# Kernel tuning notes

Hardware: AMD Instinct MI355X
Metric: run time of the kernel (lower is better)

Reference implementation:

```python
import jax, jax.numpy as jnp
import numpy as np

B, D, H, W, C = 1, 6, 128, 128, 180
NH = 6
HD = C // NH
SCALE = HD ** -0.5
WS = (2, 8, 8)
SS = (1, 4, 4)
N = WS[0] * WS[1] * WS[2]  # 128 tokens per 3D window
HID = int(C * 2.0)  # GEGLU hidden = 360


def _rel_pos_index(ws):
    d, h, w = np.meshgrid(np.arange(ws[0]), np.arange(ws[1]), np.arange(ws[2]), indexing='ij')
    coords = np.stack([d, h, w]).reshape(3, -1)  # (3, N)
    rel = (coords[:, :, None] - coords[:, None, :]).transpose(1, 2, 0).astype(np.int64)
    rel[:, :, 0] += ws[0] - 1
    rel[:, :, 1] += ws[1] - 1
    rel[:, :, 2] += ws[2] - 1
    rel[:, :, 0] *= (2 * ws[1] - 1) * (2 * ws[2] - 1)
    rel[:, :, 1] *= (2 * ws[2] - 1)
    return rel.sum(-1).astype(np.int32)  # (N, N)


def _sine_pos(hw, nf, temperature=10000.0):
    scale = 2.0 * np.pi
    ones = np.ones((1, hw[0], hw[1]), np.float64)
    y = np.cumsum(ones, 1)
    x = np.cumsum(ones, 2)
    eps = 1e-6
    y = y / (y[:, -1:, :] + eps) * scale
    x = x / (x[:, :, -1:] + eps) * scale
    dim_t = temperature ** (2 * (np.arange(nf) // 2) / nf)
    px = x[..., None] / dim_t
    py = y[..., None] / dim_t
    px = np.stack([np.sin(px[..., 0::2]), np.cos(px[..., 1::2])], -1).reshape(1, hw[0], hw[1], -1)
    py = np.stack([np.sin(py[..., 0::2]), np.cos(py[..., 1::2])], -1).reshape(1, hw[0], hw[1], -1)
    pos = np.concatenate([py, px], -1)  # (1, H, W, 2*nf)
    return pos.reshape(1, hw[0] * hw[1], -1).astype(np.float32)


def _compute_mask():
    img = np.zeros((1, D, H, W, 1), np.float32)
    cnt = 0
    sl = lambda w, s: (slice(0, -w), slice(-w, -s), slice(-s, None))
    for ds in sl(WS[0], SS[0]):
        for hs in sl(WS[1], SS[1]):
            for ws_ in sl(WS[2], SS[2]):
                img[:, ds, hs, ws_, :] = cnt
                cnt += 1
    mw = img.reshape(1, D // WS[0], WS[0], H // WS[1], WS[1], W // WS[2], WS[2], 1)
    mw = mw.transpose(0, 1, 3, 5, 2, 4, 6, 7).reshape(-1, N)
    am = mw[:, None, :] - mw[:, :, None]
    return np.where(am != 0, -100.0, 0.0).astype(np.float32)  # (nW, N, N)


def win_part(x):
    b = x.shape[0]
    x = x.reshape(b, D // WS[0], WS[0], H // WS[1], WS[1], W // WS[2], WS[2], C)
    return x.transpose(0, 1, 3, 5, 2, 4, 6, 7).reshape(-1, N, C)


def win_rev(w, b):
    x = w.reshape(b, D // WS[0], H // WS[1], W // WS[2], WS[0], WS[1], WS[2], C)
    return x.transpose(0, 1, 4, 2, 5, 3, 6, 7).reshape(b, D, H, W, C)


def ln(x, g, b):
    m = x.mean(-1, keepdims=True)
    v = ((x - m) ** 2).mean(-1, keepdims=True)
    return (x - m) / jnp.sqrt(v + 1e-5) * g + b


def attn_fn(q, k, v, bias, mask):
    # q,k,v: (B_, NH, n, HD); bias: (NH, n, n) or None; mask: (nW, n, n) or None
    a = jnp.einsum('bhnd,bhmd->bhnm', q * SCALE, k)
    if bias is not None:
        a = a + bias[None]
    if mask is not None:
        nW = mask.shape[0]
        a = a.reshape(-1, nW, NH, a.shape[-2], a.shape[-1]) + mask[None, :, None]
        a = a.reshape(-1, NH, a.shape[-2], a.shape[-1])
    a = jax.nn.softmax(a, axis=-1)
    o = jnp.einsum('bhnm,bhmd->bhnd', a, v)
    return o.transpose(0, 2, 1, 3).reshape(o.shape[0], o.shape[2], -1)


def setup_inputs() -> dict:
    key = jax.random.key(0)
    ks = jax.random.split(key, 9)
    p = lambda k, shape: jax.random.normal(k, shape, jnp.float32) * 0.02
    return {
        'x': jax.random.normal(ks[0], (B, D, H, W, C), jnp.float32),
        'mask': jnp.asarray(_compute_mask()),
        'g1': jnp.ones((C,), jnp.float32), 'b1': jnp.zeros((C,), jnp.float32),
        'g2': jnp.ones((C,), jnp.float32), 'b2': jnp.zeros((C,), jnp.float32),
        'w_qkv_self': p(ks[1], (C, 3 * C)), 'b_qkv_self': jnp.zeros((3 * C,), jnp.float32),
        'w_qkv_mut': p(ks[2], (C, 3 * C)), 'b_qkv_mut': jnp.zeros((3 * C,), jnp.float32),
        'rpb_table': p(ks[3], ((2 * WS[0] - 1) * (2 * WS[1] - 1) * (2 * WS[2] - 1), NH)),
        'pos_bias': jnp.asarray(_sine_pos((WS[1], WS[2]), C // 2)),
        'w_proj': p(ks[4], (2 * C, C)), 'b_proj': jnp.zeros((C,), jnp.float32),
        'w_fc11': p(ks[5], (C, HID)), 'b_fc11': jnp.zeros((HID,), jnp.float32),
        'w_fc12': p(ks[6], (C, HID)), 'b_fc12': jnp.zeros((HID,), jnp.float32),
        'w_fc2': p(ks[7], (HID, C)), 'b_fc2': jnp.zeros((C,), jnp.float32),
        'rpi': jnp.asarray(_rel_pos_index(WS)),
    }


def reference(x, mask, g1, b1, g2, b2, w_qkv_self, b_qkv_self, w_qkv_mut, b_qkv_mut,
              rpb_table, pos_bias, w_proj, b_proj, w_fc11, b_fc11, w_fc12, b_fc12,
              w_fc2, b_fc2, rpi):
    # --- attention branch ---
    h = ln(x, g1, b1)
    h = jnp.roll(h, (-SS[0], -SS[1], -SS[2]), axis=(1, 2, 3))  # cyclic shift
    xw = win_part(h)  # (B*nW, N, C)
    B_ = xw.shape[0]

    def qkv(xin, wq, bq):
        t = (xin @ wq + bq).reshape(B_, -1, 3, NH, HD).transpose(2, 0, 3, 1, 4)
        return t[0], t[1], t[2]

    q, k, v = qkv(xw, w_qkv_self, b_qkv_self)
    bias = rpb_table[rpi.reshape(-1)].reshape(N, N, NH).transpose(2, 0, 1)
    x_self = attn_fn(q, k, v, bias, mask)

    # mutual attention between the two frames of each window
    pb = jnp.concatenate([pos_bias, pos_bias], axis=1)  # (1, N, C)
    qm, km, vm = qkv(xw + pb, w_qkv_mut, b_qkv_mut)
    half = N // 2
    q1, q2 = qm[:, :, :half], qm[:, :, half:]
    k1, k2 = km[:, :, :half], km[:, :, half:]
    v1, v2 = vm[:, :, :half], vm[:, :, half:]
    m2 = mask[:, :half, :half]
    x1 = attn_fn(q2, k1, v1, None, m2)
    x2 = attn_fn(q1, k2, v2, None, m2)
    xo = jnp.concatenate([jnp.concatenate([x1, x2], axis=1), x_self], axis=2)  # (B_, N, 2C)
    xo = xo @ w_proj + b_proj
    out = win_rev(xo, x.shape[0])
    out = jnp.roll(out, (SS[0], SS[1], SS[2]), axis=(1, 2, 3))
    x = x + out

    # --- GEGLU MLP branch ---
    h = ln(x, g2, b2)
    h = jax.nn.gelu(h @ w_fc11 + b_fc11, approximate=False) * (h @ w_fc12 + b_fc12)
    x = x + (h @ w_fc2 + b_fc2)
    return x
```

## Files before the change

### kernel.cpp

```cpp
#include <hip/hip_runtime.h>
#include <hip/hip_bf16.h>
#include <math.h>
#include <cstdio>


typedef __hip_bfloat16 bf16;
typedef __attribute__((ext_vector_type(8))) short short8;
typedef __attribute__((ext_vector_type(4))) unsigned short us4;
typedef __attribute__((ext_vector_type(4))) float f32x4;

#define SCALE_F 0.18257418583505536f
#define SZPE 18874368u

__device__ __forceinline__ bf16  f2b(float v){ return __float2bfloat16(v); }
__device__ __forceinline__ float bu2f(unsigned short u){
    union { unsigned int i; float f; } x; x.i = ((unsigned int)u) << 16; return x.f;
}
__device__ __forceinline__ f32x4 mfma16(short8 a, short8 b, f32x4 c){
    return __builtin_amdgcn_mfma_f32_16x16x32_bf16(a, b, c, 0, 0, 0);
}

__device__ __forceinline__ void gld16(const bf16* g, bf16* s){
    __builtin_amdgcn_global_load_lds(
        (const __attribute__((address_space(1))) unsigned int*)g,
        (__attribute__((address_space(3))) unsigned int*)s, 16, 0, 0);
}

__device__ __forceinline__ int xswz(){
    return (blockIdx.x & 7) * ((int)gridDim.x >> 3) + ((int)blockIdx.x >> 3);
}

__device__ __forceinline__ int wincnt(int win, int tok){
    int d = (win >> 8) * 2 + (tok >> 6);
    int h = ((win >> 4) & 15) * 8 + ((tok >> 3) & 7);
    int w = (win & 15) * 8 + (tok & 7);
    int rd = (d >= 4) + (d >= 5);
    int rh = (h >= 120) + (h >= 124);
    int rw = (w >= 120) + (w >= 124);
    return (rd * 3 + rh) * 3 + rw;
}

__global__ __launch_bounds__(256) void k_pack_qkv(const float* __restrict__ w,
                                                  const float* __restrict__ bias,
                                                  bf16* __restrict__ Bt,
                                                  float* __restrict__ bb)
{
    int idx = blockIdx.x * 256 + threadIdx.x;
    int n = idx / 192, k = idx - n * 192;
    int three = n / 192;
    int rem = n - three * 192, nh = rem >> 5, hdp = rem & 31;
    int srcc = three * 180 + nh * 30 + hdp;
    float v = 0.f;
    if (hdp < 30 && k < 180) v = w[(size_t)k * 540 + srcc];
    if (three == 0) v *= SCALE_F;
    Bt[(size_t)n * 192 + k] = f2b(v);
    if (k == 0) bb[n] = (hdp < 30) ? ((three == 0 ? SCALE_F : 1.f) * bias[srcc]) : 0.f;
}

__global__ __launch_bounds__(256) void k_pack(const float* __restrict__ w,
                                              int NW, int K, int KP,
                                              bf16* __restrict__ Bt)
{
    int idx = blockIdx.x * 256 + threadIdx.x;
    int n = idx / KP, k = idx - n * KP;
    float v = (n < NW && k < K) ? w[(size_t)k * NW + n] : 0.f;
    Bt[idx] = f2b(v);
}

__global__ __launch_bounds__(256) void k_rpbg(const float* __restrict__ rpb,
                                              const int* __restrict__ rpi,
                                              bf16* __restrict__ biasrT)
{
    int n = blockIdx.x * 256 + threadIdx.x;
    int nh = n >> 14, rc = n & 16383;
    int row = rc >> 7, col = rc & 127;
    biasrT[((size_t)nh * 128 + col) * 128 + row] = f2b(rpb[rpi[rc] * 6 + nh]);
}

__global__ __launch_bounds__(256) void k_zpad(bf16* __restrict__ attn)
{
    int gi = blockIdx.x * 256 + threadIdx.x;
    int row = gi / 3, part = gi - row * 3;
    *(uint4*)&attn[(size_t)row * 384 + 360 + part * 8] = make_uint4(0u,0u,0u,0u);
}

template<bool ROLL_PB>
__global__ __launch_bounds__(256) void k_ln(const float* __restrict__ x,
                                            const float* __restrict__ g,
                                            const float* __restrict__ b,
                                            const float* __restrict__ pb,
                                            bf16* __restrict__ xw,
                                            bf16* __restrict__ xwm)
{
    int row  = blockIdx.x * 4 + (threadIdx.x >> 6);
    int lane = threadIdx.x & 63;
    const float* src;
    if (ROLL_PB) {
        int win = row >> 7, tok = row & 127;
        int wd = win >> 8, wh = (win >> 4) & 15, ww = win & 15;
        int td = tok >> 6, th = (tok >> 3) & 7, tw = tok & 7;
        int d = wd * 2 + td + 1; if (d >= 6) d -= 6;
        int h = (wh * 8 + th + 4) & 127;
        int w = (ww * 8 + tw + 4) & 127;
        src = x + ((size_t)((d * 128 + h) * 128 + w)) * 180;
    } else {
        src = x + (size_t)row * 180;
    }
    float v0 = src[lane];
    float v1 = src[lane + 64];
    float v2 = (lane < 52) ? src[lane + 128] : 0.f;
    float s  = v0 + v1 + v2;
    float ss = v0*v0 + v1*v1 + v2*v2;
    #pragma unroll
    for (int o = 32; o > 0; o >>= 1) { s += __shfl_xor(s, o, 64); ss += __shfl_xor(ss, o, 64); }
    float mean = s * (1.f/180.f);
    float var  = ss * (1.f/180.f) - mean*mean;
    float rstd = rsqrtf(var + 1e-5f);

    bf16* dst = xw + (size_t)row * 192;
    float y0 = (v0-mean)*rstd*g[lane]     + b[lane];
    float y1 = (v1-mean)*rstd*g[lane+64]  + b[lane+64];
    float y2 = (lane < 52) ? ((v2-mean)*rstd*g[lane+128] + b[lane+128]) : 0.f;
    dst[lane]      = f2b(y0);
    dst[lane+64]   = f2b(y1);
    if (lane < 52) dst[lane+128] = f2b(y2);
    if (lane < 12) dst[180+lane] = f2b(0.f);
    if (ROLL_PB) {
        const float* pbr = pb + (size_t)(row & 63) * 180;
        bf16* dm = xwm + (size_t)row * 192;
        dm[lane]      = f2b(y0 + pbr[lane]);
        dm[lane+64]   = f2b(y1 + pbr[lane+64]);
        if (lane < 52) dm[lane+128] = f2b(y2 + pbr[lane+128]);
        if (lane < 12) dm[180+lane] = f2b(0.f);
    }
}

template<int KP, bool DUAL>
__device__ __forceinline__ void mm2(const bf16* __restrict__ A,
                                    const bf16* __restrict__ Bt1,
                                    const bf16* __restrict__ Bt2,
                                    bf16* As, bf16* Bs1, bf16* Bs2,
                                    int m0, int n0,
                                    f32x4 (&acc1)[2][4], f32x4 (&acc2)[2][4])
{
    const int tid = threadIdx.x;
    const int w = tid >> 6, l = tid & 63, q = l >> 4, c = l & 15;
    const int lr = l >> 3, lj = l & 7;
    const int swz = ((lj ^ lr) << 3);
    #pragma unroll
    for (int ks = 0; ks < KP / 64; ks++) {
        #pragma unroll
        for (int e = 0; e < 4; e++) {
            int m = (e * 4 + w) * 8 + lr;
            gld16(&A[(size_t)(m0 + m) * KP + ks * 64 + swz], &As[((e * 4 + w) * 8) * 64]);
        }
        #pragma unroll
        for (int e = 0; e < 2; e++) {
            int n = (e * 4 + w) * 8 + lr;
            gld16(&Bt1[(size_t)(n0 + n) * KP + ks * 64 + swz], &Bs1[((e * 4 + w) * 8) * 64]);
            if (DUAL)
                gld16(&Bt2[(size_t)(n0 + n) * KP + ks * 64 + swz], &Bs2[((e * 4 + w) * 8) * 64]);
        }
        __syncthreads();
        #pragma unroll
        for (int k32 = 0; k32 < 2; k32++) {
            int koff = (((k32 * 4 + q) ^ (c & 7)) << 3);
            short8 a[2];
            #pragma unroll
            for (int mt = 0; mt < 2; mt++)
                a[mt] = *(const short8*)&As[(w * 32 + mt * 16 + c) * 64 + koff];
            #pragma unroll
            for (int nt = 0; nt < 4; nt++) {
                short8 b1 = *(const short8*)&Bs1[(nt * 16 + c) * 64 + koff];
                #pragma unroll
                for (int mt = 0; mt < 2; mt++) acc1[mt][nt] = mfma16(a[mt], b1, acc1[mt][nt]);
                if (DUAL) {
                    short8 b2 = *(const short8*)&Bs2[(nt * 16 + c) * 64 + koff];
                    #pragma unroll
                    for (int mt = 0; mt < 2; mt++) acc2[mt][nt] = mfma16(a[mt], b2, acc2[mt][nt]);
                }
            }
        }
        __syncthreads();
    }
}

__device__ __forceinline__ int cs_idx(int row, int colt){
    return row * 64 + ((((colt >> 3) ^ ((row >> 2) & 7)) << 3) | (colt & 7));
}

__global__ __launch_bounds__(256) void k_qkv(const bf16* __restrict__ A,
                                             const bf16* __restrict__ Bt,
                                             const float* __restrict__ bb,
                                             bf16* __restrict__ outq)
{
    __shared__ __align__(16) bf16 As[128 * 64];
    __shared__ __align__(16) bf16 Bs[64 * 64];
    int bid = xswz();
    int n0 = (bid % 9) * 64, m0 = (bid / 9) * 128;
    f32x4 a1[2][4] = {}, a2[2][4];
    mm2<192, false>(A, Bt, nullptr, As, Bs, nullptr, m0, n0, a1, a2);

    int tid = threadIdx.x, w = tid >> 6, l = tid & 63, q = l >> 4, c = l & 15;
    bf16* Cs = As;
    #pragma unroll
    for (int mt = 0; mt < 2; mt++)
      #pragma unroll
      for (int nt = 0; nt < 4; nt++)
        #pragma unroll
        for (int r = 0; r < 4; r++) {
            int row = w * 32 + mt * 16 + q * 4 + r;
            int colt = nt * 16 + c;
            Cs[cs_idx(row, colt)] = f2b(a1[mt][nt][r] + bb[n0 + colt]);
        }
    __syncthreads();
    int win = m0 >> 7;
    #pragma unroll
    for (int e = 0; e < 4; e++) {
        int gi = e * 256 + tid;
        int row = gi >> 3, j = gi & 7, c8 = j * 8;
        int col = n0 + c8;
        int three = col / 192, rem = col - three * 192;
        int nh = rem >> 5, hdp = rem & 31;
        bf16* dst = outq + (size_t)three * SZPE + ((size_t)(win * 6 + nh) * 128 + row) * 32 + hdp;
        *(uint4*)dst = *(const uint4*)&Cs[row * 64 + ((j ^ ((row >> 2) & 7)) << 3)];
    }
}

__global__ __launch_bounds__(256) void k_proj(const bf16* __restrict__ A,
                                              const bf16* __restrict__ Bt,
                                              const float* __restrict__ bias,
                                              const float* __restrict__ xin,
                                              float* __restrict__ res)
{
    __shared__ __align__(16) bf16 As[128 * 64];
    __shared__ __align__(16) bf16 Bs[64 * 64];
    int bid = xswz();
    int n0 = (bid % 3) * 64, m0 = (bid / 3) * 128;
    f32x4 a1[2][4] = {}, a2[2][4];
    mm2<384, false>(A, Bt, nullptr, As, Bs, nullptr, m0, n0, a1, a2);

    int w = threadIdx.x >> 6, l = threadIdx.x & 63, q = l >> 4, c = l & 15;
    #pragma unroll
    for (int mt = 0; mt < 2; mt++)
      #pragma unroll
      for (int r = 0; r < 4; r++) {
        int row = m0 + w * 32 + mt * 16 + q * 4 + r;
        int win = row >> 7, tok = row & 127;
        int wd = win >> 8, wh = (win >> 4) & 15, ww = win & 15;
        int td = tok >> 6, th = (tok >> 3) & 7, tw = tok & 7;
        int d = wd * 2 + td + 1; if (d >= 6) d -= 6;
        int h = (wh * 8 + th + 4) & 127;
        int wcol = (ww * 8 + tw + 4) & 127;
        size_t base = ((size_t)((d * 128 + h) * 128 + wcol)) * 180;
        #pragma unroll
        for (int nt = 0; nt < 4; nt++) {
            int col = n0 + nt * 16 + c;
            if (col < 180)
                res[base + col] = xin[base + col] + a1[mt][nt][r] + bias[col];
        }
      }
}

__global__ __launch_bounds__(256) void k_fc1(const bf16* __restrict__ A,
                                             const bf16* __restrict__ Bt1,
                                             const float* __restrict__ bb1,
                                             const bf16* __restrict__ Bt2,
                                             const float* __restrict__ bb2,
                                             bf16* __restrict__ hid)
{
    __shared__ __align__(16) bf16 As[128 * 64];
    __shared__ __align__(16) bf16 Bs1[64 * 64];
    __shared__ __align__(16) bf16 Bs2[64 * 64];
    int bid = xswz();
    int n0 = (bid % 6) * 64, m0 = (bid / 6) * 128;
    f32x4 a1[2][4] = {}, a2[2][4] = {};
    mm2<192, true>(A, Bt1, Bt2, As, Bs1, Bs2, m0, n0, a1, a2);

    int tid = threadIdx.x, w = tid >> 6, l = tid & 63, q = l >> 4, c = l & 15;
    bf16* Cs = As;
    #pragma unroll
    for (int mt = 0; mt < 2; mt++)
      #pragma unroll
      for (int nt = 0; nt < 4; nt++)
        #pragma unroll
        for (int r = 0; r < 4; r++) {
            int row = w * 32 + mt * 16 + q * 4 + r;
            int colt = nt * 16 + c;
            int col = n0 + colt;
            float hv = 0.f;
            if (col < 360) {
                float gate = a1[mt][nt][r] + bb1[col];
                float gl = 0.5f * gate * (1.f + erff(gate * 0.70710678118654752f));
                hv = gl * (a2[mt][nt][r] + bb2[col]);
            }
            Cs[cs_idx(row, colt)] = f2b(hv);
        }
    __syncthreads();
    #pragma unroll
    for (int e = 0; e < 4; e++) {
        int gi = e * 256 + tid;
        int row = gi >> 3, j = gi & 7, c8 = j * 8;
        *(uint4*)&hid[(size_t)(m0 + row) * 384 + n0 + c8] =
            *(const uint4*)&Cs[row * 64 + ((j ^ ((row >> 2) & 7)) << 3)];
    }
}

__global__ __launch_bounds__(256) void k_fc2(const bf16* __restrict__ A,
                                             const bf16* __restrict__ Bt,
                                             const float* __restrict__ bias,
                                             float* __restrict__ out)
{
    __shared__ __align__(16) bf16 As[128 * 64];
    __shared__ __align__(16) bf16 Bs[64 * 64];
    int bid = xswz();
    int n0 = (bid % 3) * 64, m0 = (bid / 3) * 128;
    f32x4 a1[2][4] = {}, a2[2][4];
    mm2<384, false>(A, Bt, nullptr, As, Bs, nullptr, m0, n0, a1, a2);

    int w = threadIdx.x >> 6, l = threadIdx.x & 63, q = l >> 4, c = l & 15;
    #pragma unroll
    for (int mt = 0; mt < 2; mt++)
      #pragma unroll
      for (int nt = 0; nt < 4; nt++)
        #pragma unroll
        for (int r = 0; r < 4; r++) {
            int row = m0 + w * 32 + mt * 16 + q * 4 + r;
            int col = n0 + nt * 16 + c;
            if (col < 180) {
                size_t idx = (size_t)row * 180 + col;
                out[idx] = out[idx] + a1[mt][nt][r] + bias[col];
            }
        }
}

template<bool MUT>
__global__ __launch_bounds__(256) void k_attn(const bf16* __restrict__ qkv,
                                              const bf16* __restrict__ biasrT,
                                              bf16* __restrict__ aout)
{
    __shared__ __align__(16) bf16 Vts[32 * 136];
    __shared__ __align__(16) bf16 Ps[128 * 136];

    int wh = blockIdx.x, win = wh / 6, nh = wh - win * 6;
    const bf16* qg = qkv + (size_t)wh * 4096;
    const bf16* kg = qg + (size_t)SZPE;
    const bf16* vg = qg + 2 * (size_t)SZPE;
    int tid = threadIdx.x, w = tid >> 6, l = tid & 63, q = l >> 4, c = l & 15;

    #pragma unroll
    for (int e = 0; e < 2; e++) {
        int base = (e * 256 + tid) * 8;
        int tok = base >> 5, hd0 = base & 31;
        uint4 vv = *(const uint4*)&vg[base];
        const bf16* pv = (const bf16*)&vv;
        #pragma unroll
        for (int i = 0; i < 8; i++) {
            int hd = hd0 + i;
            Vts[hd * 136 + (tok ^ (((hd >> 3) & 3) << 3))] = pv[i];
        }
    }

    f32x4 S[2][8];
    #pragma unroll
    for (int mt = 0; mt < 2; mt++)
        #pragma unroll
        for (int nt = 0; nt < 8; nt++) S[mt][nt] = (f32x4){0.f, 0.f, 0.f, 0.f};
    {
        short8 a[2];
        #pragma unroll
        for (int mt = 0; mt < 2; mt++) {
            int rq = w * 32 + mt * 16 + c;
            if (MUT) rq ^= 64;
            a[mt] = *(const short8*)&qg[rq * 32 + q * 8];
        }
        #pragma unroll
        for (int nt = 0; nt < 8; nt++) {
            short8 b = *(const short8*)&kg[(nt * 16 + c) * 32 + q * 8];
            #pragma unroll
            for (int mt = 0; mt < 2; mt++) S[mt][nt] = mfma16(a[mt], b, S[mt][nt]);
        }
    }

    int rcnt[2][4], ccnt[8];
    #pragma unroll
    for (int mt = 0; mt < 2; mt++)
        #pragma unroll
        for (int r = 0; r < 4; r++) {
            int row = w * 32 + mt * 16 + q * 4 + r;
            rcnt[mt][r] = wincnt(win, MUT ? (row & 63) : row);
        }
    #pragma unroll
    for (int nt = 0; nt < 8; nt++) {
        int col = nt * 16 + c;
        ccnt[nt] = wincnt(win, MUT ? (col & 63) : col);
    }

    float mx[2][4];
    #pragma unroll
    for (int mt = 0; mt < 2; mt++)
      #pragma unroll
      for (int r = 0; r < 4; r++) mx[mt][r] = -3.0e38f;

    #pragma unroll
    for (int mt = 0; mt < 2; mt++)
      #pragma unroll
      for (int nt = 0; nt < 8; nt++) {
        float bv[4];
        if (!MUT) {
            int col = nt * 16 + c;
            us4 bb = *(const us4*)&biasrT[((size_t)(nh * 128 + col)) * 128
                                          + w * 32 + mt * 16 + q * 4];
            #pragma unroll
            for (int r = 0; r < 4; r++) bv[r] = bu2f(bb[r]);
        }
        bool valid = (w < 2) == (nt < 4);
        #pragma unroll
        for (int r = 0; r < 4; r++) {
            float s = S[mt][nt][r];
            if (MUT) {
                s = (rcnt[mt][r] == ccnt[nt]) ? s : s - 100.f;
                s = valid ? s : -30000.f;
            } else {
                s += bv[r];
                if (rcnt[mt][r] != ccnt[nt]) s -= 100.f;
            }
            S[mt][nt][r] = s;
            mx[mt][r] = fmaxf(mx[mt][r], s);
        }
      }
    #pragma unroll
    for (int mt = 0; mt < 2; mt++)
      #pragma unroll
      for (int r = 0; r < 4; r++) {
          float m = mx[mt][r];
          #pragma unroll
          for (int o = 1; o < 16; o <<= 1) m = fmaxf(m, __shfl_xor(m, o, 64));
          mx[mt][r] = m;
      }

    float sm[2][4] = {};
    #pragma unroll
    for (int mt = 0; mt < 2; mt++)
      #pragma unroll
      for (int nt = 0; nt < 8; nt++)
        #pragma unroll
        for (int r = 0; r < 4; r++) {
            float p = __expf(S[mt][nt][r] - mx[mt][r]);
            sm[mt][r] += p;
            Ps[(w * 32 + mt * 16 + q * 4 + r) * 136 + ((nt * 16 + c) ^ (q << 3))] = f2b(p);
        }
    #pragma unroll
    for (int mt = 0; mt < 2; mt++)
      #pragma unroll
      for (int r = 0; r < 4; r++) {
          float s = sm[mt][r];
          #pragma unroll
          for (int o = 1; o < 16; o <<= 1) s += __shfl_xor(s, o, 64);
          sm[mt][r] = s;
      }
    __syncthreads();

    f32x4 O[2][2];
    #pragma unroll
    for (int mt = 0; mt < 2; mt++)
        #pragma unroll
        for (int nt = 0; nt < 2; nt++) O[mt][nt] = (f32x4){0.f, 0.f, 0.f, 0.f};
    #pragma unroll
    for (int ks = 0; ks < 4; ks++) {
        short8 a[2];
        #pragma unroll
        for (int mt = 0; mt < 2; mt++) {
            int row = w * 32 + mt * 16 + c;
            int xr = ((c >> 2) & 3) << 3;
            a[mt] = *(const short8*)&Ps[row * 136 + (ks * 32 + ((q << 3) ^ xr))];
        }
        #pragma unroll
        for (int nt = 0; nt < 2; nt++) {
            int hd = nt * 16 + c;
            int xv = ((hd >> 3) & 3) << 3;
            short8 b = *(const short8*)&Vts[hd * 136 + (ks * 32 + ((q << 3) ^ xv))];
            #pragma unroll
            for (int mt = 0; mt < 2; mt++) O[mt][nt] = mfma16(a[mt], b, O[mt][nt]);
        }
    }

    #pragma unroll
    for (int mt = 0; mt < 2; mt++)
      #pragma unroll
      for (int r = 0; r < 4; r++) {
          int row = w * 32 + mt * 16 + q * 4 + r;
          float inv = 1.f / sm[mt][r];
          #pragma unroll
          for (int nt = 0; nt < 2; nt++) {
              int col = nt * 16 + c;
              if (col < 30)
                  aout[((size_t)win * 128 + row) * 384 + (MUT ? 0 : 180) + nh * 30 + col] =
                      f2b(O[mt][nt][r] * inv);
          }
      }
}

extern "C" void kernel_launch(void* const* d_in, const int* in_sizes, int n_in,
                              void* d_out, int out_size, void* d_ws, size_t ws_size,
                              hipStream_t stream)
{
    const float* x     = (const float*)d_in[0];
    const float* mask  = (const float*)d_in[1];
    const float* g1    = (const float*)d_in[2];
    const float* b1    = (const float*)d_in[3];
    const float* g2    = (const float*)d_in[4];
    const float* b2    = (const float*)d_in[5];
    const float* wqs   = (const float*)d_in[6];
    const float* bqs   = (const float*)d_in[7];
    const float* wqm   = (const float*)d_in[8];
    const float* bqm   = (const float*)d_in[9];
    const float* rpb   = (const float*)d_in[10];
    const float* posb  = (const float*)d_in[11];
    const float* wproj = (const float*)d_in[12];
    const float* bproj = (const float*)d_in[13];
    const float* w11   = (const float*)d_in[14];
    const float* bf11  = (const float*)d_in[15];
    const float* w12   = (const float*)d_in[16];
    const float* bf12  = (const float*)d_in[17];
    const float* w2    = (const float*)d_in[18];
    const float* bf2   = (const float*)d_in[19];
    const int*   rpi   = (const int*)d_in[20];
    float* out = (float*)d_out;
    (void)mask;

    const size_t need = 265671168;
    if (ws_size < need) { fprintf(stderr, "[tmsa] ws too small: %zu < %zu\n", ws_size, need); return; }

    char* W = (char*)d_ws;
    bf16*  xw     = (bf16*)W;
    bf16*  xwm    = (bf16*)(W + 37748736);
    bf16*  attn   = (bf16*)(W + 75497472);
    bf16*  qkv    = (bf16*)(W + 150994944);
    bf16*  biasrT = (bf16*)(W + 264241152);
    bf16*  Btqs   = (bf16*)(W + 264634368);
    bf16*  Btqm   = (bf16*)(W + 264855552);
    float* bbqs   = (float*)(W + 265076736);
    float* bbqm   = (float*)(W + 265079040);
    bf16*  Btproj = (bf16*)(W + 265081344);
    bf16*  Btf11  = (bf16*)(W + 265228800);
    bf16*  Btf12  = (bf16*)(W + 265376256);
    bf16*  Btf2   = (bf16*)(W + 265523712);

    k_rpbg<<<dim3(384), 256, 0, stream>>>(rpb, rpi, biasrT);
    k_pack_qkv<<<dim3(432), 256, 0, stream>>>(wqs, bqs, Btqs, bbqs);
    k_pack_qkv<<<dim3(432), 256, 0, stream>>>(wqm, bqm, Btqm, bbqm);
    k_pack<<<dim3(288), 256, 0, stream>>>(wproj, 180, 360, 384, Btproj);
    k_pack<<<dim3(288), 256, 0, stream>>>(w11,   360, 180, 192, Btf11);
    k_pack<<<dim3(288), 256, 0, stream>>>(w12,   360, 180, 192, Btf12);
    k_pack<<<dim3(288), 256, 0, stream>>>(w2,    180, 360, 384, Btf2);

    k_ln<true><<<dim3(24576), 256, 0, stream>>>(x, g1, b1, posb, xw, xwm);
    k_zpad<<<dim3(1152), 256, 0, stream>>>(attn);
    k_qkv<<<dim3(6912), 256, 0, stream>>>(xw, Btqs, bbqs, qkv);
    k_attn<false><<<dim3(4608), 256, 0, stream>>>(qkv, biasrT, attn);
    k_qkv<<<dim3(6912), 256, 0, stream>>>(xwm, Btqm, bbqm, qkv);
    k_attn<true><<<dim3(4608), 256, 0, stream>>>(qkv, biasrT, attn);
    k_proj<<<dim3(2304), 256, 0, stream>>>(attn, Btproj, bproj, x, out);
    k_ln<false><<<dim3(24576), 256, 0, stream>>>(out, g2, b2, nullptr, xw, nullptr);
    k_fc1<<<dim3(4608), 256, 0, stream>>>(xw, Btf11, bf11, Btf12, bf12, attn);
    k_fc2<<<dim3(2304), 256, 0, stream>>>(attn, Btf2, bf2, out);
}
```

Before: 627.5 us.

## Double-buffer LDS tiles in GEMM mainloop and use fast erf approximation in GEGLU

The shared GEMM helper now loads the next K-slice into a second LDS buffer while MFMAs run on the current one. The two __syncthreads per step become one explicit vmcnt wait plus barrier, and the LDS arrays in the GEMM kernels are doubled. Separately, the GEGLU epilogue replaces erff with an Abramowitz-Stegun polynomial that uses rcp and exp, cutting transcendental cost at slightly lower accuracy. The larger LDS footprint may lower occupancy, and there are only 3 or 6 K-steps of overlap.

```diff
diff --git a/kernel.cpp b/kernel.cpp
--- a/kernel.cpp
+++ b/kernel.cpp
@@ -24,6 +24,21 @@
     __builtin_amdgcn_global_load_lds(
         (const __attribute__((address_space(1))) unsigned int*)g,
         (__attribute__((address_space(3))) unsigned int*)s, 16, 0, 0);
+}
+
+__device__ __forceinline__ void wait_vm0(){
+    asm volatile("s_waitcnt vmcnt(0)" ::: "memory");
+}
+
+__device__ __forceinline__ float gelu_erf(float x){
+    float z  = fabsf(x) * 0.70710678118654752f;
+    float t  = __builtin_amdgcn_rcpf(fmaf(0.3275911f, z, 1.f));
+    float p  = fmaf(fmaf(fmaf(fmaf(1.061405429f, t, -1.453152027f),
+                              t, 1.421413741f), t, -0.284496736f), t, 0.254829592f) * t;
+    float e  = __expf(-z * z);
+    float er = fmaf(-p, e, 1.f);
+    er = (x >= 0.f) ? er : -er;
+    return 0.5f * x * (1.f + er);
 }
 
 __device__ __forceinline__ int xswz(){
@@ -143,45 +158,67 @@
                                     int m0, int n0,
                                     f32x4 (&acc1)[2][4], f32x4 (&acc2)[2][4])
 {
+    constexpr int NS = KP / 64;
     const int tid = threadIdx.x;
     const int w = tid >> 6, l = tid & 63, q = l >> 4, c = l & 15;
     const int lr = l >> 3, lj = l & 7;
     const int swz = ((lj ^ lr) << 3);
-    #pragma unroll
-    for (int ks = 0; ks < KP / 64; ks++) {
+
+    auto stage = [&](int ks, int buf){
+        bf16* as = As + buf * (128 * 64);
         #pragma unroll
         for (int e = 0; e < 4; e++) {
             int m = (e * 4 + w) * 8 + lr;
-            gld16(&A[(size_t)(m0 + m) * KP + ks * 64 + swz], &As[((e * 4 + w) * 8) * 64]);
-        }
+            gld16(&A[(size_t)(m0 + m) * KP + ks * 64 + swz], &as[((e * 4 + w) * 8) * 64]);
+        }
+        bf16* b1 = Bs1 + buf * (64 * 64);
         #pragma unroll
         for (int e = 0; e < 2; e++) {
             int n = (e * 4 + w) * 8 + lr;
-            gld16(&Bt1[(size_t)(n0 + n) * KP + ks * 64 + swz], &Bs1[((e * 4 + w) * 8) * 64]);
-            if (DUAL)
-                gld16(&Bt2[(size_t)(n0 + n) * KP + ks * 64 + swz], &Bs2[((e * 4 + w) * 8) * 64]);
-        }
-        __syncthreads();
+            gld16(&Bt1[(size_t)(n0 + n) * KP + ks * 64 + swz], &b1[((e * 4 + w) * 8) * 64]);
+            if (DUAL) {
+                bf16* b2 = Bs2 + buf * (64 * 64);
+                gld16(&Bt2[(size_t)(n0 + n) * KP + ks * 64 + swz], &b2[((e * 4 + w) * 8) * 64]);
+            }
+        }
+    };
+
+    stage(0, 0);
+    wait_vm0();
+    __builtin_amdgcn_sched_barrier(0);
+    __builtin_amdgcn_s_barrier();
+    __builtin_amdgcn_sched_barrier(0);
+
+    #pragma unroll
+    for (int ks = 0; ks < NS; ks++) {
+        const int cur = ks & 1;
+        if (ks + 1 < NS) stage(ks + 1, cur ^ 1);
+        const bf16* as  = As  + cur * (128 * 64);
+        const bf16* b1s = Bs1 + cur * (64 * 64);
+        const bf16* b2s = DUAL ? (Bs2 + cur * (64 * 64)) : nullptr;
         #pragma unroll
         for (int k32 = 0; k32 < 2; k32++) {
             int koff = (((k32 * 4 + q) ^ (c & 7)) << 3);
             short8 a[2];
             #pragma unroll
             for (int mt = 0; mt < 2; mt++)
-                a[mt] = *(const short8*)&As[(w * 32 + mt * 16 + c) * 64 + koff];
+                a[mt] = *(const short8*)&as[(w * 32 + mt * 16 + c) * 64 + koff];
             #pragma unroll
             for (int nt = 0; nt < 4; nt++) {
-                short8 b1 = *(const short8*)&Bs1[(nt * 16 + c) * 64 + koff];
+                short8 b1 = *(const short8*)&b1s[(nt * 16 + c) * 64 + koff];
                 #pragma unroll
                 for (int mt = 0; mt < 2; mt++) acc1[mt][nt] = mfma16(a[mt], b1, acc1[mt][nt]);
                 if (DUAL) {
-                    short8 b2 = *(const short8*)&Bs2[(nt * 16 + c) * 64 + koff];
+                    short8 b2 = *(const short8*)&b2s[(nt * 16 + c) * 64 + koff];
                     #pragma unroll
                     for (int mt = 0; mt < 2; mt++) acc2[mt][nt] = mfma16(a[mt], b2, acc2[mt][nt]);
                 }
             }
         }
-        __syncthreads();
+        __builtin_amdgcn_sched_barrier(0);
+        wait_vm0();
+        __builtin_amdgcn_s_barrier();
+        __builtin_amdgcn_sched_barrier(0);
     }
 }
 
@@ -194,8 +231,8 @@
                                              const float* __restrict__ bb,
                                              bf16* __restrict__ outq)
 {
-    __shared__ __align__(16) bf16 As[128 * 64];
-    __shared__ __align__(16) bf16 Bs[64 * 64];
+    __shared__ __align__(16) bf16 As[2 * 128 * 64];
+    __shared__ __align__(16) bf16 Bs[2 * 64 * 64];
     int bid = xswz();
     int n0 = (bid % 9) * 64, m0 = (bid / 9) * 128;
     f32x4 a1[2][4] = {}, a2[2][4];
@@ -233,8 +270,8 @@
                                               const float* __restrict__ xin,
                                               float* __restrict__ res)
 {
-    __shared__ __align__(16) bf16 As[128 * 64];
-    __shared__ __align__(16) bf16 Bs[64 * 64];
+    __shared__ __align__(16) bf16 As[2 * 128 * 64];
+    __shared__ __align__(16) bf16 Bs[2 * 64 * 64];
     int bid = xswz();
     int n0 = (bid % 3) * 64, m0 = (bid / 3) * 128;
     f32x4 a1[2][4] = {}, a2[2][4];
@@ -269,9 +306,9 @@
                                              const float* __restrict__ bb2,
                                              bf16* __restrict__ hid)
 {
-    __shared__ __align__(16) bf16 As[128 * 64];
-    __shared__ __align__(16) bf16 Bs1[64 * 64];
-    __shared__ __align__(16) bf16 Bs2[64 * 64];
+    __shared__ __align__(16) bf16 As[2 * 128 * 64];
+    __shared__ __align__(16) bf16 Bs1[2 * 64 * 64];
+    __shared__ __align__(16) bf16 Bs2[2 * 64 * 64];
     int bid = xswz();
     int n0 = (bid % 6) * 64, m0 = (bid / 6) * 128;
     f32x4 a1[2][4] = {}, a2[2][4] = {};
@@ -289,11 +326,8 @@
             int colt = nt * 16 + c;
             int col = n0 + colt;
             float hv = 0.f;
-            if (col < 360) {
-                float gate = a1[mt][nt][r] + bb1[col];
-                float gl = 0.5f * gate * (1.f + erff(gate * 0.70710678118654752f));
-                hv = gl * (a2[mt][nt][r] + bb2[col]);
-            }
+            if (col < 360)
+                hv = gelu_erf(a1[mt][nt][r] + bb1[col]) * (a2[mt][nt][r] + bb2[col]);
             Cs[cs_idx(row, colt)] = f2b(hv);
         }
     __syncthreads();
@@ -311,8 +345,8 @@
                                              const float* __restrict__ bias,
                                              float* __restrict__ out)
 {
-    __shared__ __align__(16) bf16 As[128 * 64];
-    __shared__ __align__(16) bf16 Bs[64 * 64];
+    __shared__ __align__(16) bf16 As[2 * 128 * 64];
+    __shared__ __align__(16) bf16 Bs[2 * 64 * 64];
     int bid = xswz();
     int n0 = (bid % 3) * 64, m0 = (bid / 3) * 128;
     f32x4 a1[2][4] = {}, a2[2][4];
```

After: 667.3 us. +6.3%, slower.
